# Optimization experiments

Measured on AMD Instinct MI355X. Metric: run time of the kernel, lower is better.

Reference implementation:

```python
import jax, jax.numpy as jnp
import numpy as np

DIM = 768
HEADS = 12
HEAD_DIM = DIM // HEADS
SCALE = HEAD_DIM ** (-0.5)
GAMMA_INIT = 1.0


def _split_heads(x, B, H, Dh):
    # [B, N, C] -> [B, H, N, Dh]
    return x.reshape(B, -1, H, Dh).transpose(0, 2, 1, 3)


def setup_inputs() -> dict:
    key = jax.random.key(0)
    ks = jax.random.split(key, 10)
    B, N, C = 4, 1024, DIM
    w = lambda k: jax.random.normal(k, (C, C), dtype=jnp.float32) * 0.02
    return {
        "fc": jax.random.normal(ks[0], (B, N, C), dtype=jnp.float32),
        "fs": jax.random.normal(ks[1], (B, N, C), dtype=jnp.float32),
        "Wqc": w(ks[2]),
        "Wqs": w(ks[3]),
        "Wkc": w(ks[4]),
        "Wvc": w(ks[5]),
        "Wvs": w(ks[6]),
        "gamma": jnp.ones((HEADS,), dtype=jnp.float32) * GAMMA_INIT,
        "Wpc": w(ks[7]),
        "bpc": jnp.zeros((C,), dtype=jnp.float32),
        "Wps": w(ks[8]),
        "bps": jnp.zeros((C,), dtype=jnp.float32),
    }


def reference(fc, fs, Wqc, Wqs, Wkc, Wvc, Wvs, gamma, Wpc, bpc, Wps, bps):
    B, N, C = fc.shape
    H, Dh = HEADS, HEAD_DIM
    sg = jax.lax.stop_gradient

    qc = _split_heads(fc @ Wqc, B, H, Dh)
    qs = _split_heads(fs @ Wqs, B, H, Dh)
    kc = _split_heads(fc @ Wkc, B, H, Dh)
    vc = _split_heads(fc @ Wvc, B, H, Dh)
    vs = _split_heads(fs @ Wvs, B, H, Dh)

    # content attention: standard scaled QK^T
    attn_c = jnp.einsum("bhnd,bhmd->bhnm", qc, kc) * SCALE
    # semantic attention: L2-normalized self-similarity, per-head gamma
    qs_n = qs / jnp.linalg.norm(qs, axis=-1, keepdims=True)
    attn_s = jnp.einsum("bhnd,bhmd->bhnm", qs_n, qs_n) * gamma[None, :, None, None]

    # double softmax: identical forward values, asymmetric stop-gradients
    attn1 = jax.nn.softmax(attn_c + sg(attn_s), axis=-1)
    attn2 = jax.nn.softmax(sg(attn_c) + attn_s, axis=-1)

    oc = jnp.einsum("bhnm,bhmd->bhnd", attn1, vc).transpose(0, 2, 1, 3).reshape(B, N, C)
    os_ = jnp.einsum("bhnm,bhmd->bhnd", attn2, vs).transpose(0, 2, 1, 3).reshape(B, N, C)

    out_c = oc @ Wpc + bpc
    out_s = os_ @ Wps + bps
    return (out_c, out_s)
```

## Files before the change

### kernel.cpp

```cpp
#include <hip/hip_runtime.h>
#include <cstdint>
#include <cstddef>

#define DEV __device__ __forceinline__

typedef __bf16 v8bf __attribute__((ext_vector_type(8)));
typedef float v4f __attribute__((ext_vector_type(4)));
typedef uint16_t u16;

DEV u16 f2bf(float f) {
    union { __bf16 b; u16 u; } cv;
    cv.b = (__bf16)f;
    return cv.u;
}
DEV float bf2f(u16 h) { return __uint_as_float((uint32_t)h << 16); }

DEV void gload16(void* lds, const void* g) {
    __builtin_amdgcn_global_load_lds(
        (const __attribute__((address_space(1))) unsigned int*)g,
        (__attribute__((address_space(3))) unsigned int*)lds, 16, 0, 0);
}

__global__ __launch_bounds__(256) void k_cvt2(const float* __restrict__ a, const float* __restrict__ b,
                                              u16* __restrict__ da, u16* __restrict__ db) {
    const float* s = blockIdx.y ? b : a;
    u16* d = blockIdx.y ? db : da;
    int i = blockIdx.x * 256 + threadIdx.x;
    float4 v = reinterpret_cast<const float4*>(s)[i];
    ushort4 o;
    o.x = f2bf(v.x); o.y = f2bf(v.y); o.z = f2bf(v.z); o.w = f2bf(v.w);
    reinterpret_cast<ushort4*>(d)[i] = o;
}

__global__ __launch_bounds__(256) void k_transpose_w(
    const float* __restrict__ w0, const float* __restrict__ w1, const float* __restrict__ w2,
    const float* __restrict__ w3, const float* __restrict__ w4, const float* __restrict__ w5,
    const float* __restrict__ w6, u16* __restrict__ Wt) {
    __shared__ float tl[32][33];
    const float* W;
    switch (blockIdx.z) {
        case 0: W = w0; break; case 1: W = w1; break; case 2: W = w2; break;
        case 3: W = w3; break; case 4: W = w4; break; case 5: W = w5; break;
        default: W = w6; break;
    }
    int n0 = blockIdx.x * 32, k0 = blockIdx.y * 32;
    int tx = threadIdx.x & 31, ty = threadIdx.x >> 5;
    #pragma unroll
    for (int i = 0; i < 4; ++i)
        tl[ty + i*8][tx] = W[(size_t)(k0 + ty + i*8) * 768 + n0 + tx];
    __syncthreads();
    u16* O = Wt + (size_t)blockIdx.z * 589824;
    #pragma unroll
    for (int i = 0; i < 4; ++i)
        O[(size_t)(n0 + ty + i*8) * 768 + k0 + tx] = f2bf(tl[tx][ty + i*8]);
}

DEV void gemm_main(const u16* __restrict__ A, const u16* __restrict__ W,
                   u16* As, u16* Bs, int m0, int n0, v4f acc[4][4]) {
    const int t = threadIdx.x, lane = t & 63;
    const int wid = t >> 6, wm = wid >> 1, wn = wid & 1;
    const int lr = lane & 15, kg = lane >> 4;
    const int lrow = lane >> 3, lslot = lane & 7;
    const int s = lslot ^ lrow;
    #pragma unroll
    for (int mi = 0; mi < 4; ++mi)
        #pragma unroll
        for (int ni = 0; ni < 4; ++ni) acc[mi][ni] = (v4f){0.f, 0.f, 0.f, 0.f};
    for (int kt = 0; kt < 12; ++kt) {
        int k0 = kt * 64;
        #pragma unroll
        for (int c = 0; c < 4; ++c) {
            int rb = wid * 32 + c * 8;
            int r = rb + lrow;
            gload16((char*)As + rb * 128, A + (size_t)(m0 + r) * 768 + k0 + s * 8);
            gload16((char*)Bs + rb * 128, W + (size_t)(n0 + r) * 768 + k0 + s * 8);
        }
        __syncthreads();
        #pragma unroll
        for (int kk = 0; kk < 2; ++kk) {
            int kb2 = (kk * 32 + kg * 8) * 2;
            v8bf af[4], bfr[4];
            #pragma unroll
            for (int mi = 0; mi < 4; ++mi) {
                int rr = wm * 64 + mi * 16 + lr;
                af[mi] = *reinterpret_cast<const v8bf*>(reinterpret_cast<const char*>(As) + rr * 128 + (kb2 ^ ((rr & 7) << 4)));
            }
            #pragma unroll
            for (int ni = 0; ni < 4; ++ni) {
                int rr = wn * 64 + ni * 16 + lr;
                bfr[ni] = *reinterpret_cast<const v8bf*>(reinterpret_cast<const char*>(Bs) + rr * 128 + (kb2 ^ ((rr & 7) << 4)));
            }
            #pragma unroll
            for (int mi = 0; mi < 4; ++mi)
                #pragma unroll
                for (int ni = 0; ni < 4; ++ni)
                    acc[mi][ni] = __builtin_amdgcn_mfma_f32_16x16x32_bf16(af[mi], bfr[ni], acc[mi][ni], 0, 0, 0);
        }
        __syncthreads();
    }
}

__global__ __launch_bounds__(256) void k_gemm_proj(
    const u16* __restrict__ fcb, const u16* __restrict__ fsb, const u16* __restrict__ Wt,
    u16* __restrict__ qc, u16* __restrict__ kc, u16* __restrict__ vc,
    u16* __restrict__ qs, u16* __restrict__ vs) {
    __shared__ __align__(16) u16 As[8192], Bs[8192];
    const u16* A; const u16* W; u16* O;
    switch (blockIdx.z) {
        case 0:  A = fcb; W = Wt;              O = qc; break;
        case 1:  A = fcb; W = Wt + 589824;     O = kc; break;
        case 2:  A = fcb; W = Wt + 2 * 589824; O = vc; break;
        case 3:  A = fsb; W = Wt + 3 * 589824; O = qs; break;
        default: A = fsb; W = Wt + 4 * 589824; O = vs; break;
    }
    int m0 = blockIdx.y * 128, n0 = blockIdx.x * 128;
    v4f acc[4][4];
    gemm_main(A, W, As, Bs, m0, n0, acc);
    const int lane = threadIdx.x & 63, wid = threadIdx.x >> 6;
    const int wm = wid >> 1, wn = wid & 1, lr = lane & 15, kg = lane >> 4;
    if (blockIdx.z == 0) {
        #pragma unroll
        for (int mi = 0; mi < 4; ++mi)
            #pragma unroll
            for (int ni = 0; ni < 4; ++ni)
                #pragma unroll
                for (int r = 0; r < 4; ++r) acc[mi][ni][r] *= 0.18033688f;
    } else if (blockIdx.z == 3) {
        #pragma unroll
        for (int mi = 0; mi < 4; ++mi)
            #pragma unroll
            for (int r = 0; r < 4; ++r) {
                float ss = 0.f;
                #pragma unroll
                for (int ni = 0; ni < 4; ++ni) ss += acc[mi][ni][r] * acc[mi][ni][r];
                ss += __shfl_xor(ss, 1); ss += __shfl_xor(ss, 2);
                ss += __shfl_xor(ss, 4); ss += __shfl_xor(ss, 8);
                float rs = rsqrtf(ss);
                #pragma unroll
                for (int ni = 0; ni < 4; ++ni) acc[mi][ni][r] *= rs;
            }
    }
    #pragma unroll
    for (int mi = 0; mi < 4; ++mi)
        #pragma unroll
        for (int ni = 0; ni < 4; ++ni)
            #pragma unroll
            for (int r = 0; r < 4; ++r) {
                int rowg = m0 + wm * 64 + mi * 16 + kg * 4 + r;
                int colg = n0 + wn * 64 + ni * 16 + lr;
                O[(size_t)rowg * 768 + colg] = f2bf(acc[mi][ni][r]);
            }
}

__global__ __launch_bounds__(256) void k_gemm_out(
    const u16* __restrict__ ocb, const u16* __restrict__ osb, const u16* __restrict__ Wt,
    const float* __restrict__ bpc, const float* __restrict__ bps, float* __restrict__ out) {
    __shared__ __align__(16) u16 As[8192], Bs[8192];
    const u16* A; const u16* W; const float* bias; float* O;
    if (blockIdx.z == 0) { A = ocb; W = Wt + 5 * 589824; bias = bpc; O = out; }
    else                 { A = osb; W = Wt + 6 * 589824; bias = bps; O = out + 3145728; }
    int m0 = blockIdx.y * 128, n0 = blockIdx.x * 128;
    v4f acc[4][4];
    gemm_main(A, W, As, Bs, m0, n0, acc);
    const int lane = threadIdx.x & 63, wid = threadIdx.x >> 6;
    const int wm = wid >> 1, wn = wid & 1, lr = lane & 15, kg = lane >> 4;
    #pragma unroll
    for (int mi = 0; mi < 4; ++mi)
        #pragma unroll
        for (int ni = 0; ni < 4; ++ni)
            #pragma unroll
            for (int r = 0; r < 4; ++r) {
                int rowg = m0 + wm * 64 + mi * 16 + kg * 4 + r;
                int colg = n0 + wn * 64 + ni * 16 + lr;
                O[(size_t)rowg * 768 + colg] = acc[mi][ni][r] + bias[colg];
            }
}

__global__ __launch_bounds__(256) void k_transpose_v(
    const u16* __restrict__ vc, const u16* __restrict__ vs,
    u16* __restrict__ vcT, u16* __restrict__ vsT) {
    __shared__ u16 tile[64][65];
    const u16* src = blockIdx.z ? vs : vc;
    u16* dst = blockIdx.z ? vsT : vcT;
    int bh = blockIdx.y, b = bh / 12, h = bh % 12;
    int n0 = blockIdx.x * 64;
    int t = threadIdx.x;
    #pragma unroll
    for (int i = 0; i < 16; ++i) {
        int idx = i * 256 + t, n = idx >> 6, d = idx & 63;
        tile[n][d] = src[(size_t)(b * 1024 + n0 + n) * 768 + h * 64 + d];
    }
    __syncthreads();
    #pragma unroll
    for (int i = 0; i < 16; ++i) {
        int idx = i * 256 + t, d = idx >> 6, n = idx & 63;
        dst[(size_t)(bh * 64 + d) * 1024 + n0 + n] = tile[n][d];
    }
}

__global__ __launch_bounds__(256) void k_attn(
    const u16* __restrict__ qc, const u16* __restrict__ kc, const u16* __restrict__ qsn,
    const u16* __restrict__ vcT, const u16* __restrict__ vsT,
    const float* __restrict__ gamma,
    u16* __restrict__ oc, u16* __restrict__ os) {
    __shared__ __align__(16) u16 KQ[2][4][4096];
    __shared__ __align__(16) u16 P_s[4096];
    const int t = threadIdx.x, lane = t & 63, w = t >> 6;
    const int lr = lane & 15, kg = lane >> 4;
    const int lrow = lane >> 3, lslot = lane & 7;
    const int sslot = lslot ^ lrow;

    int lin = blockIdx.y * 16 + blockIdx.x;
    int swz = (lin & 7) * 96 + (lin >> 3);
    const int qb = swz & 15, bh = swz >> 4;
    const int b = bh / 12, h = bh % 12;
    const float gam = gamma[h] * 1.44269504088896340736f;

    const u16* gb; size_t rstride, kmul;
    switch (w) {
        case 0:  gb = kc  + (size_t)b * 786432 + h * 64; rstride = 768;  kmul = 768; break;
        case 1:  gb = qsn + (size_t)b * 786432 + h * 64; rstride = 768;  kmul = 768; break;
        case 2:  gb = vcT + (size_t)bh * 65536;          rstride = 1024; kmul = 1;   break;
        default: gb = vsT + (size_t)bh * 65536;          rstride = 1024; kmul = 1;   break;
    }

    int qrow = qb * 64 + w * 16 + lr;
    const u16* q1p = qc  + (size_t)(b * 1024 + qrow) * 768 + h * 64 + kg * 8;
    const u16* q2p = qsn + (size_t)(b * 1024 + qrow) * 768 + h * 64 + kg * 8;
    v8bf qcA[2], qsA[2];
    qcA[0] = *reinterpret_cast<const v8bf*>(q1p);
    qcA[1] = *reinterpret_cast<const v8bf*>(q1p + 32);
    qsA[0] = *reinterpret_cast<const v8bf*>(q2p);
    qsA[1] = *reinterpret_cast<const v8bf*>(q2p + 32);

    v4f oAcc[4], sAcc[4];
    #pragma unroll
    for (int i = 0; i < 4; ++i) { oAcc[i] = (v4f){0.f,0.f,0.f,0.f}; sAcc[i] = (v4f){0.f,0.f,0.f,0.f}; }
    float l_i[4] = {0.f, 0.f, 0.f, 0.f};

    {
        char* ld = (char*)KQ[0][w];
        #pragma unroll
        for (int c = 0; c < 8; ++c) {
            int r = c * 8 + lrow;
            gload16(ld + c * 1024, gb + (size_t)r * rstride + sslot * 8);
        }
    }
    __syncthreads();

    int cur = 0;
    for (int tile = 0; tile < 16; ++tile) {
        if (tile < 15) {
            size_t kv1 = (size_t)(tile + 1) * 64;
            char* ld = (char*)KQ[cur ^ 1][w];
            #pragma unroll
            for (int c = 0; c < 8; ++c) {
                int r = c * 8 + lrow;
                gload16(ld + c * 1024, gb + kv1 * kmul + (size_t)r * rstride + sslot * 8);
            }
        }
        const char* K_s  = (const char*)KQ[cur][0];
        const char* Q2_s = (const char*)KQ[cur][1];
        const char* Vc_s = (const char*)KQ[cur][2];
        const char* Vs_s = (const char*)KQ[cur][3];

        v4f sc[4], ss_[4];
        __builtin_amdgcn_s_setprio(1);
        #pragma unroll
        for (int cb = 0; cb < 4; ++cb) {
            int kr = cb * 16 + lr;
            v4f ac = {0.f,0.f,0.f,0.f}, as = {0.f,0.f,0.f,0.f};
            #pragma unroll
            for (int kk = 0; kk < 2; ++kk) {
                int kb2 = (kk * 32 + kg * 8) * 2;
                int off = kr * 128 + (kb2 ^ ((kr & 7) << 4));
                v8bf kf  = *reinterpret_cast<const v8bf*>(K_s + off);
                v8bf q2f = *reinterpret_cast<const v8bf*>(Q2_s + off);
                ac = __builtin_amdgcn_mfma_f32_16x16x32_bf16(qcA[kk], kf,  ac, 0, 0, 0);
                as = __builtin_amdgcn_mfma_f32_16x16x32_bf16(qsA[kk], q2f, as, 0, 0, 0);
            }
            sc[cb] = ac; ss_[cb] = as;
        }
        __builtin_amdgcn_s_setprio(0);

        float pv[4][4];
        #pragma unroll
        for (int cb = 0; cb < 4; ++cb)
            #pragma unroll
            for (int r = 0; r < 4; ++r) {
                float p = __builtin_exp2f(fmaf(gam, ss_[cb][r], sc[cb][r]));
                pv[cb][r] = p;
                l_i[r] += p;
            }

        #pragma unroll
        for (int cb = 0; cb < 4; ++cb)
            #pragma unroll
            for (int r = 0; r < 4; ++r) {
                int prow = kg * 4 + r, pcol = cb * 16 + lr;
                int off = w * 2048 + prow * 128 + ((pcol * 2) ^ ((prow & 7) << 4));
                *reinterpret_cast<u16*>(reinterpret_cast<char*>(P_s) + off) = f2bf(pv[cb][r]);
            }

        __builtin_amdgcn_s_setprio(1);
        #pragma unroll
        for (int kk = 0; kk < 2; ++kk) {
            int kb2 = (kk * 32 + kg * 8) * 2;
            int poff = w * 2048 + lr * 128 + (kb2 ^ ((lr & 7) << 4));
            v8bf ap = *reinterpret_cast<const v8bf*>(reinterpret_cast<const char*>(P_s) + poff);
            #pragma unroll
            for (int db = 0; db < 4; ++db) {
                int vr = db * 16 + lr;
                int voff = vr * 128 + (kb2 ^ ((vr & 7) << 4));
                v8bf vcf = *reinterpret_cast<const v8bf*>(Vc_s + voff);
                v8bf vsf = *reinterpret_cast<const v8bf*>(Vs_s + voff);
                oAcc[db] = __builtin_amdgcn_mfma_f32_16x16x32_bf16(ap, vcf, oAcc[db], 0, 0, 0);
                sAcc[db] = __builtin_amdgcn_mfma_f32_16x16x32_bf16(ap, vsf, sAcc[db], 0, 0, 0);
            }
        }
        __builtin_amdgcn_s_setprio(0);

        __syncthreads();
        cur ^= 1;
    }

    #pragma unroll
    for (int r = 0; r < 4; ++r) {
        float l = l_i[r];
        l += __shfl_xor(l, 1); l += __shfl_xor(l, 2);
        l += __shfl_xor(l, 4); l += __shfl_xor(l, 8);
        float rl = 1.0f / l;
        int qg = qb * 64 + w * 16 + kg * 4 + r;
        size_t base = (size_t)(b * 1024 + qg) * 768 + h * 64;
        #pragma unroll
        for (int db = 0; db < 4; ++db) {
            oc[base + db * 16 + lr] = f2bf(oAcc[db][r] * rl);
            os[base + db * 16 + lr] = f2bf(sAcc[db][r] * rl);
        }
    }
}

extern "C" void kernel_launch(void* const* d_in, const int* in_sizes, int n_in,
                              void* d_out, int out_size, void* d_ws, size_t ws_size,
                              hipStream_t stream) {
    const float* fc    = (const float*)d_in[0];
    const float* fs    = (const float*)d_in[1];
    const float* Wqc   = (const float*)d_in[2];
    const float* Wqs   = (const float*)d_in[3];
    const float* Wkc   = (const float*)d_in[4];
    const float* Wvc   = (const float*)d_in[5];
    const float* Wvs   = (const float*)d_in[6];
    const float* gamma = (const float*)d_in[7];
    const float* Wpc   = (const float*)d_in[8];
    const float* bpc   = (const float*)d_in[9];
    const float* Wps   = (const float*)d_in[10];
    const float* bps   = (const float*)d_in[11];
    float* out = (float*)d_out;

    const size_t NT = 3145728;
    u16* ws  = (u16*)d_ws;
    u16* fcb = ws;
    u16* fsb = fcb + NT;
    u16* Wt  = fsb + NT;
    u16* qc  = Wt + (size_t)7 * 589824;
    u16* kc  = qc + NT;
    u16* vc  = kc + NT;
    u16* qs  = vc + NT;
    u16* vs  = qs + NT;
    u16* vcT = vs + NT;
    u16* vsT = vcT + NT;
    u16* ocb = fcb;
    u16* osb = fsb;

    k_cvt2<<<dim3(3072, 2), 256, 0, stream>>>(fc, fs, fcb, fsb);
    k_transpose_w<<<dim3(24, 24, 7), 256, 0, stream>>>(Wqc, Wkc, Wvc, Wqs, Wvs, Wpc, Wps, Wt);
    k_gemm_proj<<<dim3(6, 32, 5), 256, 0, stream>>>(fcb, fsb, Wt, qc, kc, vc, qs, vs);
    k_transpose_v<<<dim3(16, 48, 2), 256, 0, stream>>>(vc, vs, vcT, vsT);
    k_attn<<<dim3(16, 48), 256, 0, stream>>>(qc, kc, qs, vcT, vsT, gamma, ocb, osb);
    k_gemm_out<<<dim3(6, 32, 2), 256, 0, stream>>>(ocb, osb, Wt, bpc, bps, out);
}
```

Before: 138.3 us.

## Switch attention to 32x32x16 MFMA with register-resident P and split-KV warps

The attention kernel now uses 32x32x16 bf16 MFMA instead of 16x16x32. S is computed transposed so the probability tile stays in registers, and bf16 pairs are exchanged with cross-half lane shuffles instead of passing through an LDS P buffer. Each pair of waves splits the KV tile across 32 query rows, and the partial outputs and row sums are combined through LDS at the end. Launch bounds request two blocks per CU. This removes the P_s LDS round trip and the extra instruction count of the smaller MFMA, at the cost of a final LDS reduction, higher register pressure, and a __syncthreads before the reduction-buffer reuse.

Measured after the change: 127.3 us. -7.9%, faster.

```diff
diff --git a/kernel.cpp b/kernel.cpp
--- a/kernel.cpp
+++ b/kernel.cpp
@@ -6,6 +6,7 @@
 
 typedef __bf16 v8bf __attribute__((ext_vector_type(8)));
 typedef float v4f __attribute__((ext_vector_type(4)));
+typedef float f32x16 __attribute__((ext_vector_type(16)));
 typedef uint16_t u16;
 
 DEV u16 f2bf(float f) {
@@ -14,6 +15,13 @@
     return cv.u;
 }
 DEV float bf2f(u16 h) { return __uint_as_float((uint32_t)h << 16); }
+
+DEV uint32_t pkbf(float a, float b) {
+    typedef __bf16 bf2v __attribute__((ext_vector_type(2)));
+    union { bf2v v; uint32_t u; } c;
+    c.v = (bf2v){(__bf16)a, (__bf16)b};
+    return c.u;
+}
 
 DEV void gload16(void* lds, const void* g) {
     __builtin_amdgcn_global_load_lds(
@@ -198,15 +206,15 @@
     }
 }
 
-__global__ __launch_bounds__(256) void k_attn(
+__global__ __launch_bounds__(256, 2) void k_attn(
     const u16* __restrict__ qc, const u16* __restrict__ kc, const u16* __restrict__ qsn,
     const u16* __restrict__ vcT, const u16* __restrict__ vsT,
     const float* __restrict__ gamma,
     u16* __restrict__ oc, u16* __restrict__ os) {
     __shared__ __align__(16) u16 KQ[2][4][4096];
-    __shared__ __align__(16) u16 P_s[4096];
     const int t = threadIdx.x, lane = t & 63, w = t >> 6;
-    const int lr = lane & 15, kg = lane >> 4;
+    const int lq = lane & 31, hf = lane >> 5;
+    const int qg = w >> 1, kvh = w & 1;
     const int lrow = lane >> 3, lslot = lane & 7;
     const int sslot = lslot ^ lrow;
 
@@ -224,19 +232,22 @@
         default: gb = vsT + (size_t)bh * 65536;          rstride = 1024; kmul = 1;   break;
     }
 
-    int qrow = qb * 64 + w * 16 + lr;
-    const u16* q1p = qc  + (size_t)(b * 1024 + qrow) * 768 + h * 64 + kg * 8;
-    const u16* q2p = qsn + (size_t)(b * 1024 + qrow) * 768 + h * 64 + kg * 8;
-    v8bf qcA[2], qsA[2];
-    qcA[0] = *reinterpret_cast<const v8bf*>(q1p);
-    qcA[1] = *reinterpret_cast<const v8bf*>(q1p + 32);
-    qsA[0] = *reinterpret_cast<const v8bf*>(q2p);
-    qsA[1] = *reinterpret_cast<const v8bf*>(q2p + 32);
-
-    v4f oAcc[4], sAcc[4];
-    #pragma unroll
-    for (int i = 0; i < 4; ++i) { oAcc[i] = (v4f){0.f,0.f,0.f,0.f}; sAcc[i] = (v4f){0.f,0.f,0.f,0.f}; }
-    float l_i[4] = {0.f, 0.f, 0.f, 0.f};
+    const u16* qp1 = qc  + (size_t)(b * 1024 + qb * 64 + qg * 32 + lq) * 768 + h * 64 + hf * 8;
+    const u16* qp2 = qsn + (size_t)(b * 1024 + qb * 64 + qg * 32 + lq) * 768 + h * 64 + hf * 8;
+    v8bf qcB[4], qsB[4];
+    #pragma unroll
+    for (int s = 0; s < 4; ++s) {
+        qcB[s] = *reinterpret_cast<const v8bf*>(qp1 + s * 16);
+        qsB[s] = *reinterpret_cast<const v8bf*>(qp2 + s * 16);
+    }
+
+    f32x16 ocA[2], osA[2];
+    #pragma unroll
+    for (int dt = 0; dt < 2; ++dt) {
+        #pragma unroll
+        for (int r = 0; r < 16; ++r) { ocA[dt][r] = 0.f; osA[dt][r] = 0.f; }
+    }
+    float lsum = 0.f;
 
     {
         char* ld = (char*)KQ[0][w];
@@ -264,58 +275,66 @@
         const char* Vc_s = (const char*)KQ[cur][2];
         const char* Vs_s = (const char*)KQ[cur][3];
 
-        v4f sc[4], ss_[4];
+        f32x16 ac, as;
+        #pragma unroll
+        for (int r = 0; r < 16; ++r) { ac[r] = 0.f; as[r] = 0.f; }
+        const int rowA = kvh * 32 + lq;
         __builtin_amdgcn_s_setprio(1);
         #pragma unroll
-        for (int cb = 0; cb < 4; ++cb) {
-            int kr = cb * 16 + lr;
-            v4f ac = {0.f,0.f,0.f,0.f}, as = {0.f,0.f,0.f,0.f};
-            #pragma unroll
-            for (int kk = 0; kk < 2; ++kk) {
-                int kb2 = (kk * 32 + kg * 8) * 2;
-                int off = kr * 128 + (kb2 ^ ((kr & 7) << 4));
-                v8bf kf  = *reinterpret_cast<const v8bf*>(K_s + off);
-                v8bf q2f = *reinterpret_cast<const v8bf*>(Q2_s + off);
-                ac = __builtin_amdgcn_mfma_f32_16x16x32_bf16(qcA[kk], kf,  ac, 0, 0, 0);
-                as = __builtin_amdgcn_mfma_f32_16x16x32_bf16(qsA[kk], q2f, as, 0, 0, 0);
-            }
-            sc[cb] = ac; ss_[cb] = as;
+        for (int s = 0; s < 4; ++s) {
+            int colb = s * 32 + hf * 16;
+            int off = rowA * 128 + (colb ^ ((rowA & 7) << 4));
+            v8bf kf  = *reinterpret_cast<const v8bf*>(K_s + off);
+            v8bf q2f = *reinterpret_cast<const v8bf*>(Q2_s + off);
+            ac = __builtin_amdgcn_mfma_f32_32x32x16_bf16(kf,  qcB[s], ac, 0, 0, 0);
+            as = __builtin_amdgcn_mfma_f32_32x32x16_bf16(q2f, qsB[s], as, 0, 0, 0);
         }
         __builtin_amdgcn_s_setprio(0);
 
-        float pv[4][4];
-        #pragma unroll
-        for (int cb = 0; cb < 4; ++cb)
-            #pragma unroll
-            for (int r = 0; r < 4; ++r) {
-                float p = __builtin_exp2f(fmaf(gam, ss_[cb][r], sc[cb][r]));
-                pv[cb][r] = p;
-                l_i[r] += p;
-            }
-
-        #pragma unroll
-        for (int cb = 0; cb < 4; ++cb)
-            #pragma unroll
-            for (int r = 0; r < 4; ++r) {
-                int prow = kg * 4 + r, pcol = cb * 16 + lr;
-                int off = w * 2048 + prow * 128 + ((pcol * 2) ^ ((prow & 7) << 4));
-                *reinterpret_cast<u16*>(reinterpret_cast<char*>(P_s) + off) = f2bf(pv[cb][r]);
-            }
+        float p[16];
+        #pragma unroll
+        for (int r = 0; r < 16; ++r)
+            p[r] = __builtin_exp2f(fmaf(gam, as[r], ac[r]));
+        lsum += ((p[0]+p[1])+(p[2]+p[3])) + ((p[4]+p[5])+(p[6]+p[7]))
+              + ((p[8]+p[9])+(p[10]+p[11])) + ((p[12]+p[13])+(p[14]+p[15]));
+
+        uint32_t A0 = pkbf(p[0], p[1]),  A1 = pkbf(p[2], p[3]);
+        uint32_t A2 = pkbf(p[4], p[5]),  A3 = pkbf(p[6], p[7]);
+        uint32_t A4 = pkbf(p[8], p[9]),  A5 = pkbf(p[10], p[11]);
+        uint32_t A6 = pkbf(p[12], p[13]), A7 = pkbf(p[14], p[15]);
+        uint32_t pay0 = hf ? A0 : A2;
+        uint32_t pay1 = hf ? A1 : A3;
+        uint32_t rec0 = (uint32_t)__shfl_xor((int)pay0, 32);
+        uint32_t rec1 = (uint32_t)__shfl_xor((int)pay1, 32);
+        uint32_t w0 = hf ? rec0 : A0;
+        uint32_t w1 = hf ? rec1 : A1;
+        uint32_t w2 = hf ? A2 : rec0;
+        uint32_t w3 = hf ? A3 : rec1;
+        uint32_t pay2 = hf ? A4 : A6;
+        uint32_t pay3 = hf ? A5 : A7;
+        uint32_t rec2 = (uint32_t)__shfl_xor((int)pay2, 32);
+        uint32_t rec3 = (uint32_t)__shfl_xor((int)pay3, 32);
+        uint32_t w4 = hf ? rec2 : A4;
+        uint32_t w5 = hf ? rec3 : A5;
+        uint32_t w6 = hf ? A6 : rec2;
+        uint32_t w7 = hf ? A7 : rec3;
+        union { uint32_t u[4]; v8bf v; } pa0, pa1;
+        pa0.u[0] = w0; pa0.u[1] = w1; pa0.u[2] = w2; pa0.u[3] = w3;
+        pa1.u[0] = w4; pa1.u[1] = w5; pa1.u[2] = w6; pa1.u[3] = w7;
 
         __builtin_amdgcn_s_setprio(1);
         #pragma unroll
-        for (int kk = 0; kk < 2; ++kk) {
-            int kb2 = (kk * 32 + kg * 8) * 2;
-            int poff = w * 2048 + lr * 128 + (kb2 ^ ((lr & 7) << 4));
-            v8bf ap = *reinterpret_cast<const v8bf*>(reinterpret_cast<const char*>(P_s) + poff);
-            #pragma unroll
-            for (int db = 0; db < 4; ++db) {
-                int vr = db * 16 + lr;
-                int voff = vr * 128 + (kb2 ^ ((vr & 7) << 4));
-                v8bf vcf = *reinterpret_cast<const v8bf*>(Vc_s + voff);
-                v8bf vsf = *reinterpret_cast<const v8bf*>(Vs_s + voff);
-                oAcc[db] = __builtin_amdgcn_mfma_f32_16x16x32_bf16(ap, vcf, oAcc[db], 0, 0, 0);
-                sAcc[db] = __builtin_amdgcn_mfma_f32_16x16x32_bf16(ap, vsf, sAcc[db], 0, 0, 0);
+        for (int dt = 0; dt < 2; ++dt) {
+            int rowV = dt * 32 + lq;
+            #pragma unroll
+            for (int s = 0; s < 2; ++s) {
+                int colb = kvh * 64 + s * 32 + hf * 16;
+                int off = rowV * 128 + (colb ^ ((rowV & 7) << 4));
+                v8bf vcf = *reinterpret_cast<const v8bf*>(Vc_s + off);
+                v8bf vsf = *reinterpret_cast<const v8bf*>(Vs_s + off);
+                v8bf ap = s ? pa1.v : pa0.v;
+                ocA[dt] = __builtin_amdgcn_mfma_f32_32x32x16_bf16(ap, vcf, ocA[dt], 0, 0, 0);
+                osA[dt] = __builtin_amdgcn_mfma_f32_32x32x16_bf16(ap, vsf, osA[dt], 0, 0, 0);
             }
         }
         __builtin_amdgcn_s_setprio(0);
@@ -324,19 +343,42 @@
         cur ^= 1;
     }
 
-    #pragma unroll
-    for (int r = 0; r < 4; ++r) {
-        float l = l_i[r];
-        l += __shfl_xor(l, 1); l += __shfl_xor(l, 2);
-        l += __shfl_xor(l, 4); l += __shfl_xor(l, 8);
-        float rl = 1.0f / l;
-        int qg = qb * 64 + w * 16 + kg * 4 + r;
-        size_t base = (size_t)(b * 1024 + qg) * 768 + h * 64;
-        #pragma unroll
-        for (int db = 0; db < 4; ++db) {
-            oc[base + db * 16 + lr] = f2bf(oAcc[db][r] * rl);
-            os[base + db * 16 + lr] = f2bf(sAcc[db][r] * rl);
-        }
+    lsum += __shfl_xor(lsum, 32);
+    float* red   = reinterpret_cast<float*>(&KQ[0][0][0]);
+    float* red_l = red;
+    float* red_o = red + 64;
+    if (kvh == 1) {
+        if (lane < 32) red_l[qg * 32 + lq] = lsum;
+        #pragma unroll
+        for (int st = 0; st < 2; ++st)
+            #pragma unroll
+            for (int dt = 0; dt < 2; ++dt)
+                #pragma unroll
+                for (int r = 0; r < 16; ++r) {
+                    int idx = st * 32 + dt * 16 + r;
+                    float v = st ? osA[dt][r] : ocA[dt][r];
+                    red_o[(qg * 64 + idx) * 64 + lane] = v;
+                }
+    }
+    __syncthreads();
+    if (kvh == 0) {
+        float ltot = lsum + red_l[qg * 32 + lq];
+        float rl = 1.0f / ltot;
+        if (lane < 32) red_l[qg * 32 + lq] = rl;
+        #pragma unroll
+        for (int st = 0; st < 2; ++st)
+            #pragma unroll
+            for (int dt = 0; dt < 2; ++dt)
+                #pragma unroll
+                for (int r = 0; r < 16; ++r) {
+                    int rowq = (r & 3) + 8 * (r >> 2) + 4 * hf;
+                    float rlv = red_l[qg * 32 + rowq];
+                    int idx = st * 32 + dt * 16 + r;
+                    float own = st ? osA[dt][r] : ocA[dt][r];
+                    float v = (own + red_o[(qg * 64 + idx) * 64 + lane]) * rlv;
+                    u16* dst = st ? os : oc;
+                    dst[(size_t)(b * 1024 + qb * 64 + qg * 32 + rowq) * 768 + h * 64 + dt * 32 + lq] = f2bf(v);
+                }
     }
 }
 
```
